# Kernel tuning notes

Measured on AMD Instinct MI355X. Metric: run time of the kernel, lower is better.

Reference implementation:

```python
import jax, jax.numpy as jnp
import numpy as np

B, T, N, C_IN, C_OUT, CHEB_K, ST_EMB = 8, 12, 2048, 64, 64, 2, 64


def setup_inputs() -> dict:
    key = jax.random.key(0)
    ks = jax.random.split(key, 9)
    inv = 1.0 / np.sqrt(ST_EMB)
    return {
        "x": jax.random.normal(ks[0], (B, T, N, C_IN), dtype=jnp.float32),
        "adj": jax.random.uniform(ks[1], (N, N), dtype=jnp.float32),
        "st_emb": jax.random.normal(ks[2], (T, 1, ST_EMB), dtype=jnp.float32),
        "weights": jax.random.normal(ks[3], (CHEB_K, C_IN, C_OUT), dtype=jnp.float32) * 0.02,
        "bias": jax.random.normal(ks[4], (C_OUT,), dtype=jnp.float32) * 0.02,
        "W1": jax.random.uniform(ks[5], (ST_EMB, 32), minval=-inv, maxval=inv, dtype=jnp.float32),
        "b1": jax.random.uniform(ks[6], (32,), minval=-inv, maxval=inv, dtype=jnp.float32),
        "W2": jax.random.uniform(ks[7], (32, 1), minval=-1/np.sqrt(32), maxval=1/np.sqrt(32), dtype=jnp.float32),
        "b2": jax.random.uniform(ks[8], (1,), minval=-1/np.sqrt(32), maxval=1/np.sqrt(32), dtype=jnp.float32),
    }


def reference(x, adj, st_emb, weights, bias, W1, b1, W2, b2):
    # lambda MLP: Linear -> ReLU -> Linear, then 1 + relu(.)
    h = jax.nn.relu(st_emb @ W1 + b1)            # [T,1,32]
    lam = 1.0 + jax.nn.relu(h @ W2 + b2)         # [T,1,1]
    c1 = (2.0 * lam - 2.0) / lam                 # [T,1,1] diagonal-scale coefficient
    c2 = 2.0 / lam                               # [T,1,1]
    # identity support einsum == per-time diagonal scaling of x
    x_g1 = c1[None] * x                          # [B,T,N,C]
    # adjacency support: scale factored out of the N x N contraction
    x_g2 = c2[None] * jnp.einsum('nm,btmc->btnc', adj, x)  # [B,T,N,C]
    x_g = jnp.stack([x_g1, x_g2], axis=3)        # [B,T,N,K,C]
    return jnp.einsum('btnki,kio->btno', x_g, weights) + bias
```

## Files before the change

kernel.cpp:

```cpp
#include <hip/hip_runtime.h>
#include <hip/hip_bf16.h>

#define B_ 8
#define T_ 12
#define N_ 2048
#define C_ 64
#define BM 128
#define BK 64

typedef __attribute__((ext_vector_type(4))) float f32x4;
typedef __attribute__((ext_vector_type(4))) __bf16 bf16x4;
typedef __attribute__((ext_vector_type(8))) __bf16 bf16x8;

#define GAS __attribute__((address_space(1)))
#define LAS __attribute__((address_space(3)))

static __device__ __forceinline__ void gld_lds16(const void* g, void* l) {
    __builtin_amdgcn_global_load_lds((const GAS void*)g, (LAS void*)l, 16, 0, 0);
}

#define WS_CBUF 0
#define WS_WTB  1024
#define WS_ADJB 32768
#define WS_XT   (32768 + 8388608)
#define WS_NEED ((size_t)(WS_XT) + 25165824)

__global__ void lam_kernel(const float* __restrict__ st, const float* __restrict__ W1,
                           const float* __restrict__ b1, const float* __restrict__ W2,
                           const float* __restrict__ b2, float* __restrict__ cbuf) {
    const int t = threadIdx.x >> 5;
    const int h = threadIdx.x & 31;
    if (t >= T_) return;
    float acc = b1[h];
    #pragma unroll 8
    for (int e = 0; e < 64; ++e) acc += st[t * 64 + e] * W1[e * 32 + h];
    float hv = fmaxf(acc, 0.f) * W2[h];
    #pragma unroll
    for (int off = 16; off; off >>= 1) hv += __shfl_down(hv, off, 32);
    if (h == 0) {
        float lam = 1.f + fmaxf(hv + b2[0], 0.f);
        cbuf[t]      = 2.f - 2.f / lam;
        cbuf[T_ + t] = 2.f / lam;
    }
}

__global__ void lamw_kernel(const float* __restrict__ st, const float* __restrict__ W1,
                            const float* __restrict__ b1, const float* __restrict__ W2,
                            const float* __restrict__ b2, const float* __restrict__ weights,
                            float* __restrict__ cbuf, __bf16* __restrict__ WtB) {
    const int t = threadIdx.x >> 5;
    const int h = threadIdx.x & 31;
    if (t < T_) {
        float acc = b1[h];
        #pragma unroll 8
        for (int e = 0; e < 64; ++e) acc += st[t * 64 + e] * W1[e * 32 + h];
        float hv = fmaxf(acc, 0.f) * W2[h];
        #pragma unroll
        for (int off = 16; off; off >>= 1) hv += __shfl_down(hv, off, 32);
        if (h == 0) {
            float lam = 1.f + fmaxf(hv + b2[0], 0.f);
            cbuf[t]      = 2.f - 2.f / lam;
            cbuf[T_ + t] = 2.f / lam;
        }
    }
    for (int e = threadIdx.x; e < 64 * 128; e += 512) {
        int o = e >> 7, k = e & 127;
        float v = (k < 64) ? weights[4096 + k * 64 + o] : weights[(k - 64) * 64 + o];
        WtB[o * 128 + k] = (__bf16)v;
    }
}

__global__ void cvt_fused(const float* __restrict__ x, __bf16* __restrict__ xT,
                          const float* __restrict__ adj, __bf16* __restrict__ adjb) {
    const int bid = blockIdx.x;
    const int tid = threadIdx.x;
    if (bid >= 3072) {
        const size_t i = ((size_t)(bid - 3072) * 256 + tid) * 8;
        const float4 f0 = *(const float4*)&adj[i];
        const float4 f1 = *(const float4*)&adj[i + 4];
        bf16x8 h = { (__bf16)f0.x, (__bf16)f0.y, (__bf16)f0.z, (__bf16)f0.w,
                     (__bf16)f1.x, (__bf16)f1.y, (__bf16)f1.z, (__bf16)f1.w };
        *(bf16x8*)&adjb[i] = h;
        return;
    }
    __shared__ __align__(16) __bf16 t[64][72];
    const int bt = bid >> 5, n0 = (bid & 31) * 64;
    {
        const int r = tid >> 2, c0 = (tid & 3) * 16;
        const float* src = x + ((size_t)bt * N_ + n0 + r) * C_ + c0;
        #pragma unroll
        for (int i = 0; i < 4; ++i) {
            float4 f = *(const float4*)(src + 4 * i);
            t[c0 + 4 * i + 0][r] = (__bf16)f.x;
            t[c0 + 4 * i + 1][r] = (__bf16)f.y;
            t[c0 + 4 * i + 2][r] = (__bf16)f.z;
            t[c0 + 4 * i + 3][r] = (__bf16)f.w;
        }
    }
    __syncthreads();
    {
        const int c = tid >> 2, nf = (tid & 3) * 16;
        __bf16* dst = xT + ((size_t)bt * C_ + c) * N_ + n0 + nf;
        *(bf16x8*)(dst)     = *(const bf16x8*)&t[c][nf];
        *(bf16x8*)(dst + 8) = *(const bf16x8*)&t[c][nf + 8];
    }
}

__global__ __launch_bounds__(256, 2) void dgcn_main2(
    const __bf16* __restrict__ adjb, const __bf16* __restrict__ xT,
    const float* __restrict__ x, const __bf16* __restrict__ WtB,
    const float* __restrict__ bias, const float* __restrict__ cbuf,
    float* __restrict__ out)
{
    __shared__ __align__(16) __bf16 smem[32768];
    char* sb = (char*)smem;

    const int m0  = blockIdx.x * BM;
    const int btg = blockIdx.y;
    const int tid = threadIdx.x;
    const int l   = tid & 63, w = tid >> 6;
    const int wr  = w >> 1, wc = w & 1;
    const int lr  = l & 15, lk = l >> 4;

    const __bf16* srcA[4];
    const __bf16* srcB[4];
    #pragma unroll
    for (int i = 0; i < 4; ++i) {
        int s = (w * 4 + i) * 64 + l;
        int r = s >> 3, j = s & 7;
        srcA[i] = adjb + (size_t)(m0 + r) * N_ + 8 * (j ^ (r & 7));
        int bb = s >> 9, c = (s >> 3) & 63;
        srcB[i] = xT + ((size_t)(btg * 2 + bb) * C_ + c) * N_ + 8 * (j ^ (c & 7));
    }

    f32x4 acc[4][4] = {};

    #pragma unroll
    for (int i = 0; i < 4; ++i) {
        gld_lds16(srcA[i], sb + (w * 4 + i) * 1024);
        gld_lds16(srcB[i], sb + 16384 + (w * 4 + i) * 1024);
    }

    int sel = 0;
    for (int kt = 0; kt < N_ / BK; ++kt) {
        __syncthreads();
        if (kt < N_ / BK - 1) {
            const int wo = (sel ^ 1) * 32768;
            #pragma unroll
            for (int i = 0; i < 4; ++i) {
                srcA[i] += BK;
                srcB[i] += BK;
                gld_lds16(srcA[i], sb + wo + (w * 4 + i) * 1024);
                gld_lds16(srcB[i], sb + wo + 16384 + (w * 4 + i) * 1024);
            }
        }
        const char* base = sb + sel * 32768;
        #pragma unroll
        for (int ks = 0; ks < 2; ++ks) {
            const int kb = ks * 64 + lk * 16;
            bf16x8 a[4];
            #pragma unroll
            for (int mi = 0; mi < 4; ++mi) {
                int rr = wr * 64 + mi * 16 + lr;
                a[mi] = *(const bf16x8*)(base + rr * 128 + (kb ^ ((rr & 7) << 4)));
            }
            #pragma unroll
            for (int nj = 0; nj < 4; ++nj) {
                int cc = nj * 16 + lr;
                bf16x8 b = *(const bf16x8*)(base + 16384 + wc * 8192 + cc * 128 + (kb ^ ((cc & 7) << 4)));
                #pragma unroll
                for (int mi = 0; mi < 4; ++mi)
                    acc[mi][nj] = __builtin_amdgcn_mfma_f32_16x16x32_bf16(a[mi], b, acc[mi][nj], 0, 0, 0);
            }
        }
        sel ^= 1;
    }

    #pragma unroll
    for (int bb = 0; bb < 2; ++bb) {
        const int btA = btg * 2 + bb;
        const int tloc = btA % T_;
        const float c1 = cbuf[tloc];
        const float c2 = cbuf[T_ + tloc];
        __syncthreads();
        if (wc == bb) {
            #pragma unroll
            for (int mi = 0; mi < 4; ++mi)
                #pragma unroll
                for (int nj = 0; nj < 4; ++nj)
                    #pragma unroll
                    for (int q = 0; q < 4; ++q) {
                        int row = wr * 64 + mi * 16 + lk * 4 + q;
                        int colb = (nj * 16 + lr) * 2;
                        *(__bf16*)(sb + row * 256 + (colb ^ ((row & 7) << 4))) =
                            (__bf16)(c2 * acc[mi][nj][q]);
                    }
        }
        {
            int row = w * 32 + (l >> 1);
            int c0 = (l & 1) * 32;
            const float* xs = x + ((size_t)btA * N_ + m0 + row) * C_ + c0;
            #pragma unroll
            for (int i = 0; i < 4; ++i) {
                float4 f0 = *(const float4*)(xs + 8 * i);
                float4 f1 = *(const float4*)(xs + 8 * i + 4);
                bf16x8 h = { (__bf16)(c1 * f0.x), (__bf16)(c1 * f0.y),
                             (__bf16)(c1 * f0.z), (__bf16)(c1 * f0.w),
                             (__bf16)(c1 * f1.x), (__bf16)(c1 * f1.y),
                             (__bf16)(c1 * f1.z), (__bf16)(c1 * f1.w) };
                int colb = 128 + c0 * 2 + 16 * i;
                *(bf16x8*)(sb + row * 256 + (colb ^ ((row & 7) << 4))) = h;
            }
        }
        __syncthreads();
        f32x4 oacc[2][4] = {};
        #pragma unroll
        for (int ks = 0; ks < 4; ++ks) {
            const int kb = ks * 64 + lk * 16;
            bf16x8 ea[2];
            #pragma unroll
            for (int mi2 = 0; mi2 < 2; ++mi2) {
                int row = w * 32 + mi2 * 16 + lr;
                ea[mi2] = *(const bf16x8*)(sb + row * 256 + (kb ^ ((row & 7) << 4)));
            }
            #pragma unroll
            for (int nj = 0; nj < 4; ++nj) {
                int o = nj * 16 + lr;
                bf16x8 bw = *(const bf16x8*)(WtB + o * 128 + ks * 32 + lk * 8);
                oacc[0][nj] = __builtin_amdgcn_mfma_f32_16x16x32_bf16(ea[0], bw, oacc[0][nj], 0, 0, 0);
                oacc[1][nj] = __builtin_amdgcn_mfma_f32_16x16x32_bf16(ea[1], bw, oacc[1][nj], 0, 0, 0);
            }
        }
        float* ob = out + (size_t)btA * N_ * C_;
        #pragma unroll
        for (int nj = 0; nj < 4; ++nj) {
            const float bv = bias[nj * 16 + lr];
            #pragma unroll
            for (int mi2 = 0; mi2 < 2; ++mi2)
                #pragma unroll
                for (int q = 0; q < 4; ++q) {
                    int row = w * 32 + mi2 * 16 + lk * 4 + q;
                    ob[(size_t)(m0 + row) * C_ + nj * 16 + lr] = oacc[mi2][nj][q] + bv;
                }
        }
    }
}

#define LDM 72
#define LDE 136
__global__ __launch_bounds__(256, 3) void dgcn_fb(
    const float* __restrict__ x, const float* __restrict__ adj,
    const float* __restrict__ weights, const float* __restrict__ bias,
    const float* __restrict__ cbuf, float* __restrict__ out)
{
    __shared__ __align__(16) __bf16 smem[BM * LDE];
    __shared__ __align__(16) __bf16 Wt[64 * LDE];
    __bf16* As = smem;
    __bf16* Bs = smem + BM * LDM;
    __bf16* E  = smem;

    const int mtile = blockIdx.x;
    const int bt    = blockIdx.y;
    const int tloc  = bt % T_;
    const int m0    = mtile * BM;
    const int tid   = threadIdx.x;
    const int lane  = tid & 63;
    const int w     = tid >> 6;

    const float c1 = cbuf[tloc];
    const float c2 = cbuf[T_ + tloc];
    const float* xbt = x + (size_t)bt * N_ * C_;

    for (int e = tid; e < 2 * 64 * 64; e += 256) {
        int kk = e >> 6, o = e & 63;
        float v = (kk < 64) ? weights[4096 + kk * 64 + o] : weights[(kk - 64) * 64 + o];
        Wt[o * LDE + kk] = (__bf16)v;
    }

    f32x4 acc[2][4] = {};
    const int c4 = tid & 15;
    const int rg = tid >> 4;
    const int lr = lane & 15;
    const int lk = lane >> 4;

    for (int kt = 0; kt < N_ / BK; ++kt) {
        const int k0 = kt * BK;
        __syncthreads();
        #pragma unroll
        for (int j = 0; j < 8; ++j) {
            const int r = rg + 16 * j;
            const float4 f = *(const float4*)&adj[(size_t)(m0 + r) * N_ + k0 + 4 * c4];
            bf16x4 h = { (__bf16)f.x, (__bf16)f.y, (__bf16)f.z, (__bf16)f.w };
            *(bf16x4*)&As[r * LDM + 4 * c4] = h;
        }
        #pragma unroll
        for (int j = 0; j < 4; ++j) {
            const int k  = (tid & 15) + 16 * j;
            const int c0 = 4 * (tid >> 4);
            const float4 f = *(const float4*)&xbt[(size_t)(k0 + k) * C_ + c0];
            Bs[(c0 + 0) * LDM + k] = (__bf16)f.x;
            Bs[(c0 + 1) * LDM + k] = (__bf16)f.y;
            Bs[(c0 + 2) * LDM + k] = (__bf16)f.z;
            Bs[(c0 + 3) * LDM + k] = (__bf16)f.w;
        }
        __syncthreads();
        #pragma unroll
        for (int ks = 0; ks < 2; ++ks) {
            bf16x8 a0 = *(const bf16x8*)&As[(w * 32 +  0 + lr) * LDM + ks * 32 + lk * 8];
            bf16x8 a1 = *(const bf16x8*)&As[(w * 32 + 16 + lr) * LDM + ks * 32 + lk * 8];
            #pragma unroll
            for (int nj = 0; nj < 4; ++nj) {
                bf16x8 b = *(const bf16x8*)&Bs[(nj * 16 + lr) * LDM + ks * 32 + lk * 8];
                acc[0][nj] = __builtin_amdgcn_mfma_f32_16x16x32_bf16(a0, b, acc[0][nj], 0, 0, 0);
                acc[1][nj] = __builtin_amdgcn_mfma_f32_16x16x32_bf16(a1, b, acc[1][nj], 0, 0, 0);
            }
        }
    }
    __syncthreads();

    #pragma unroll
    for (int j = 0; j < 8; ++j) {
        const int r = rg + 16 * j;
        const float4 f = *(const float4*)&xbt[(size_t)(m0 + r) * C_ + 4 * c4];
        bf16x4 h = { (__bf16)(c1 * f.x), (__bf16)(c1 * f.y), (__bf16)(c1 * f.z), (__bf16)(c1 * f.w) };
        *(bf16x4*)&E[r * LDE + 64 + 4 * c4] = h;
    }
    #pragma unroll
    for (int mi = 0; mi < 2; ++mi)
        #pragma unroll
        for (int nj = 0; nj < 4; ++nj)
            #pragma unroll
            for (int q = 0; q < 4; ++q) {
                const int row = w * 32 + mi * 16 + lk * 4 + q;
                const int col = nj * 16 + lr;
                E[row * LDE + col] = (__bf16)(c2 * acc[mi][nj][q]);
            }
    __syncthreads();

    f32x4 oacc[2][4] = {};
    #pragma unroll
    for (int ks = 0; ks < 4; ++ks) {
        bf16x8 a0 = *(const bf16x8*)&E[(w * 32 +  0 + lr) * LDE + ks * 32 + lk * 8];
        bf16x8 a1 = *(const bf16x8*)&E[(w * 32 + 16 + lr) * LDE + ks * 32 + lk * 8];
        #pragma unroll
        for (int nj = 0; nj < 4; ++nj) {
            bf16x8 bw = *(const bf16x8*)&Wt[(nj * 16 + lr) * LDE + ks * 32 + lk * 8];
            oacc[0][nj] = __builtin_amdgcn_mfma_f32_16x16x32_bf16(a0, bw, oacc[0][nj], 0, 0, 0);
            oacc[1][nj] = __builtin_amdgcn_mfma_f32_16x16x32_bf16(a1, bw, oacc[1][nj], 0, 0, 0);
        }
    }
    float* obt = out + (size_t)bt * N_ * C_;
    #pragma unroll
    for (int nj = 0; nj < 4; ++nj) {
        const float bv = bias[nj * 16 + lr];
        #pragma unroll
        for (int mi = 0; mi < 2; ++mi)
            #pragma unroll
            for (int q = 0; q < 4; ++q) {
                const int row = w * 32 + mi * 16 + lk * 4 + q;
                obt[(size_t)(m0 + row) * C_ + nj * 16 + lr] = oacc[mi][nj][q] + bv;
            }
    }
}

extern "C" void kernel_launch(void* const* d_in, const int* in_sizes, int n_in,
                              void* d_out, int out_size, void* d_ws, size_t ws_size,
                              hipStream_t stream) {
    const float* x       = (const float*)d_in[0];
    const float* adj     = (const float*)d_in[1];
    const float* st_emb  = (const float*)d_in[2];
    const float* weights = (const float*)d_in[3];
    const float* bias    = (const float*)d_in[4];
    const float* W1      = (const float*)d_in[5];
    const float* b1      = (const float*)d_in[6];
    const float* W2      = (const float*)d_in[7];
    const float* b2      = (const float*)d_in[8];
    float* out = (float*)d_out;
    char* ws = (char*)d_ws;
    float* cbuf = (float*)(ws + WS_CBUF);

    if (ws_size >= WS_NEED) {
        __bf16* WtB  = (__bf16*)(ws + WS_WTB);
        __bf16* adjb = (__bf16*)(ws + WS_ADJB);
        __bf16* xT   = (__bf16*)(ws + WS_XT);
        lamw_kernel<<<1, 512, 0, stream>>>(st_emb, W1, b1, W2, b2, weights, cbuf, WtB);
        cvt_fused<<<5120, 256, 0, stream>>>(x, xT, adj, adjb);
        dgcn_main2<<<dim3(N_ / BM, B_ * T_ / 2), 256, 0, stream>>>(adjb, xT, x, WtB, bias, cbuf, out);
    } else {
        lam_kernel<<<1, 384, 0, stream>>>(st_emb, W1, b1, W2, b2, cbuf);
        dgcn_fb<<<dim3(N_ / BM, B_ * T_), 256, 0, stream>>>(x, adj, weights, bias, cbuf, out);
    }
}
```

Baseline: 99.15 us.

## Reassociate graph conv: apply weights before adjacency GEMM, fuse epilogue

Uses associativity to compute P1 = x·W1 and P0 = c1·x·W0 + bias in the conversion kernel, so the large adjacency GEMM multiplies adj by the projected P1 (stored transposed in bf16) and the epilogue simply adds c2·acc to P0. This removes the second per-tile MFMA stage and the LDS staging of the concatenated feature tile. The main GEMM now covers three bt slices per block (N=192) with a larger LDS buffer, and P0 is held in bf16 or fp32 depending on workspace size. The trade-off is extra rounding from bf16 P1 and P0, plus a larger LDS footprint that may reduce occupancy.

```diff
diff --git a/kernel.cpp b/kernel.cpp
--- a/kernel.cpp
+++ b/kernel.cpp
@@ -22,8 +22,10 @@
 #define WS_CBUF 0
 #define WS_WTB  1024
 #define WS_ADJB 32768
-#define WS_XT   (32768 + 8388608)
-#define WS_NEED ((size_t)(WS_XT) + 25165824)
+#define WS_P1T  (32768 + 8388608)
+#define WS_P0S  (WS_P1T + 25165824)
+#define WS_MID  ((size_t)WS_P0S)
+#define WS_FULL ((size_t)WS_P0S + 25165824)
 
 __global__ void lam_kernel(const float* __restrict__ st, const float* __restrict__ W1,
                            const float* __restrict__ b1, const float* __restrict__ W2,
@@ -70,12 +72,17 @@
     }
 }
 
-__global__ void cvt_fused(const float* __restrict__ x, __bf16* __restrict__ xT,
-                          const float* __restrict__ adj, __bf16* __restrict__ adjb) {
+template<bool FULLP>
+__global__ __launch_bounds__(256, 4) void pcvt_kernel(
+    const float* __restrict__ x, const float* __restrict__ adj,
+    const __bf16* __restrict__ WtB, const float* __restrict__ cbuf,
+    const float* __restrict__ bias, __bf16* __restrict__ adjb,
+    __bf16* __restrict__ P1T, __bf16* __restrict__ P0S, float* __restrict__ out)
+{
     const int bid = blockIdx.x;
     const int tid = threadIdx.x;
-    if (bid >= 3072) {
-        const size_t i = ((size_t)(bid - 3072) * 256 + tid) * 8;
+    if (bid >= 1536) {
+        const size_t i = ((size_t)(bid - 1536) * 256 + tid) * 8;
         const float4 f0 = *(const float4*)&adj[i];
         const float4 f1 = *(const float4*)&adj[i + 4];
         bf16x8 h = { (__bf16)f0.x, (__bf16)f0.y, (__bf16)f0.z, (__bf16)f0.w,
@@ -83,36 +90,81 @@
         *(bf16x8*)&adjb[i] = h;
         return;
     }
-    __shared__ __align__(16) __bf16 t[64][72];
-    const int bt = bid >> 5, n0 = (bid & 31) * 64;
-    {
-        const int r = tid >> 2, c0 = (tid & 3) * 16;
-        const float* src = x + ((size_t)bt * N_ + n0 + r) * C_ + c0;
-        #pragma unroll
-        for (int i = 0; i < 4; ++i) {
-            float4 f = *(const float4*)(src + 4 * i);
-            t[c0 + 4 * i + 0][r] = (__bf16)f.x;
-            t[c0 + 4 * i + 1][r] = (__bf16)f.y;
-            t[c0 + 4 * i + 2][r] = (__bf16)f.z;
-            t[c0 + 4 * i + 3][r] = (__bf16)f.w;
-        }
+    __shared__ __align__(16) __bf16 T[64 * 128];
+    char* TB = (char*)T;
+    const int bt = bid >> 4, n0 = (bid & 15) * 128;
+    const int l = tid & 63, w = tid >> 6;
+    const int lr = l & 15, lk = l >> 4;
+    const float c1 = cbuf[bt % T_];
+
+    f32x4 p1[2][4] = {}, p0[2][4] = {};
+    #pragma unroll
+    for (int ks = 0; ks < 2; ++ks) {
+        bf16x8 a[2];
+        #pragma unroll
+        for (int mi = 0; mi < 2; ++mi) {
+            const float* xs = x + ((size_t)bt * N_ + n0 + w * 32 + mi * 16 + lr) * C_ + ks * 32 + lk * 8;
+            float4 f0 = *(const float4*)xs;
+            float4 f1 = *(const float4*)(xs + 4);
+            a[mi] = { (__bf16)f0.x, (__bf16)f0.y, (__bf16)f0.z, (__bf16)f0.w,
+                      (__bf16)f1.x, (__bf16)f1.y, (__bf16)f1.z, (__bf16)f1.w };
+        }
+        #pragma unroll
+        for (int nj = 0; nj < 4; ++nj) {
+            const __bf16* wb = WtB + (nj * 16 + lr) * 128 + ks * 32 + lk * 8;
+            bf16x8 b1v = *(const bf16x8*)wb;
+            bf16x8 b0v = *(const bf16x8*)(wb + 64);
+            #pragma unroll
+            for (int mi = 0; mi < 2; ++mi) {
+                p1[mi][nj] = __builtin_amdgcn_mfma_f32_16x16x32_bf16(a[mi], b1v, p1[mi][nj], 0, 0, 0);
+                p0[mi][nj] = __builtin_amdgcn_mfma_f32_16x16x32_bf16(a[mi], b0v, p0[mi][nj], 0, 0, 0);
+            }
+        }
+    }
+    #pragma unroll
+    for (int nj = 0; nj < 4; ++nj) {
+        const int o = nj * 16 + lr;
+        const float bv = bias[o];
+        #pragma unroll
+        for (int mi = 0; mi < 2; ++mi)
+            #pragma unroll
+            for (int q = 0; q < 4; ++q) {
+                const int row = w * 32 + mi * 16 + lk * 4 + q;
+                const size_t idx = ((size_t)bt * N_ + n0 + row) * C_ + o;
+                const float v = c1 * p0[mi][nj][q] + bv;
+                if (FULLP) P0S[idx] = (__bf16)v; else out[idx] = v;
+            }
+    }
+    #pragma unroll
+    for (int nj = 0; nj < 4; ++nj) {
+        const int o = nj * 16 + lr;
+        #pragma unroll
+        for (int mi = 0; mi < 2; ++mi)
+            #pragma unroll
+            for (int q = 0; q < 4; ++q) {
+                const int row = w * 32 + mi * 16 + lk * 4 + q;
+                *(__bf16*)(TB + o * 256 + ((row * 2) ^ ((o & 7) << 4))) = (__bf16)p1[mi][nj][q];
+            }
     }
     __syncthreads();
     {
-        const int c = tid >> 2, nf = (tid & 3) * 16;
-        __bf16* dst = xT + ((size_t)bt * C_ + c) * N_ + n0 + nf;
-        *(bf16x8*)(dst)     = *(const bf16x8*)&t[c][nf];
-        *(bf16x8*)(dst + 8) = *(const bf16x8*)&t[c][nf + 8];
-    }
-}
-
-__global__ __launch_bounds__(256, 2) void dgcn_main2(
-    const __bf16* __restrict__ adjb, const __bf16* __restrict__ xT,
-    const float* __restrict__ x, const __bf16* __restrict__ WtB,
-    const float* __restrict__ bias, const float* __restrict__ cbuf,
+        const int o = tid >> 2, seg = tid & 3;
+        __bf16* dst = P1T + ((size_t)bt * 64 + o) * N_ + n0 + seg * 32;
+        #pragma unroll
+        for (int i = 0; i < 4; ++i) {
+            const int chunk = seg * 64 + i * 16;
+            *(bf16x8*)(dst + i * 8) = *(const bf16x8*)(TB + o * 256 + (chunk ^ ((o & 7) << 4)));
+        }
+    }
+}
+
+template<bool FULLP>
+__global__ __launch_bounds__(256, 2) void dgcn_main3(
+    const __bf16* __restrict__ adjb, const __bf16* __restrict__ P1T,
+    const __bf16* __restrict__ P0S, const float* __restrict__ cbuf,
     float* __restrict__ out)
 {
-    __shared__ __align__(16) __bf16 smem[32768];
+    __shared__ __align__(16) __bf16 smem[40960];
     char* sb = (char*)smem;
 
     const int m0  = blockIdx.x * BM;
@@ -123,38 +175,45 @@
     const int lr  = l & 15, lk = l >> 4;
 
     const __bf16* srcA[4];
-    const __bf16* srcB[4];
+    const __bf16* srcB[6];
     #pragma unroll
     for (int i = 0; i < 4; ++i) {
         int s = (w * 4 + i) * 64 + l;
         int r = s >> 3, j = s & 7;
         srcA[i] = adjb + (size_t)(m0 + r) * N_ + 8 * (j ^ (r & 7));
-        int bb = s >> 9, c = (s >> 3) & 63;
-        srcB[i] = xT + ((size_t)(btg * 2 + bb) * C_ + c) * N_ + 8 * (j ^ (c & 7));
-    }
-
-    f32x4 acc[4][4] = {};
-
-    #pragma unroll
-    for (int i = 0; i < 4; ++i) {
-        gld_lds16(srcA[i], sb + (w * 4 + i) * 1024);
-        gld_lds16(srcB[i], sb + 16384 + (w * 4 + i) * 1024);
-    }
+    }
+    #pragma unroll
+    for (int i = 0; i < 6; ++i) {
+        int s = (w * 6 + i) * 64 + l;
+        int btl = s >> 9, rem = s & 511;
+        int o = rem >> 3, j = rem & 7;
+        srcB[i] = P1T + ((size_t)(btg * 3 + btl) * 64 + o) * N_ + 8 * (j ^ (o & 7));
+    }
+
+    f32x4 acc[4][6] = {};
+
+    #pragma unroll
+    for (int i = 0; i < 4; ++i) gld_lds16(srcA[i], sb + (w * 4 + i) * 1024);
+    #pragma unroll
+    for (int i = 0; i < 6; ++i) gld_lds16(srcB[i], sb + 16384 + (w * 6 + i) * 1024);
 
     int sel = 0;
     for (int kt = 0; kt < N_ / BK; ++kt) {
         __syncthreads();
         if (kt < N_ / BK - 1) {
-            const int wo = (sel ^ 1) * 32768;
+            const int wo = (sel ^ 1) * 40960;
             #pragma unroll
             for (int i = 0; i < 4; ++i) {
                 srcA[i] += BK;
+                gld_lds16(srcA[i], sb + wo + (w * 4 + i) * 1024);
+            }
+            #pragma unroll
+            for (int i = 0; i < 6; ++i) {
                 srcB[i] += BK;
-                gld_lds16(srcA[i], sb + wo + (w * 4 + i) * 1024);
-                gld_lds16(srcB[i], sb + wo + 16384 + (w * 4 + i) * 1024);
-            }
-        }
-        const char* base = sb + sel * 32768;
+                gld_lds16(srcB[i], sb + wo + 16384 + (w * 6 + i) * 1024);
+            }
+        }
+        const char* base = sb + sel * 40960;
         #pragma unroll
         for (int ks = 0; ks < 2; ++ks) {
             const int kb = ks * 64 + lk * 16;
@@ -165,9 +224,10 @@
                 a[mi] = *(const bf16x8*)(base + rr * 128 + (kb ^ ((rr & 7) << 4)));
             }
             #pragma unroll
-            for (int nj = 0; nj < 4; ++nj) {
-                int cc = nj * 16 + lr;
-                bf16x8 b = *(const bf16x8*)(base + 16384 + wc * 8192 + cc * 128 + (kb ^ ((cc & 7) << 4)));
+            for (int nj = 0; nj < 6; ++nj) {
+                int c = wc * 96 + nj * 16 + lr;
+                int btl = c >> 6, o = c & 63;
+                bf16x8 b = *(const bf16x8*)(base + 16384 + btl * 8192 + o * 128 + (kb ^ ((o & 7) << 4)));
                 #pragma unroll
                 for (int mi = 0; mi < 4; ++mi)
                     acc[mi][nj] = __builtin_amdgcn_mfma_f32_16x16x32_bf16(a[mi], b, acc[mi][nj], 0, 0, 0);
@@ -177,72 +237,20 @@
     }
 
     #pragma unroll
-    for (int bb = 0; bb < 2; ++bb) {
-        const int btA = btg * 2 + bb;
-        const int tloc = btA % T_;
-        const float c1 = cbuf[tloc];
-        const float c2 = cbuf[T_ + tloc];
-        __syncthreads();
-        if (wc == bb) {
-            #pragma unroll
-            for (int mi = 0; mi < 4; ++mi)
-                #pragma unroll
-                for (int nj = 0; nj < 4; ++nj)
-                    #pragma unroll
-                    for (int q = 0; q < 4; ++q) {
-                        int row = wr * 64 + mi * 16 + lk * 4 + q;
-                        int colb = (nj * 16 + lr) * 2;
-                        *(__bf16*)(sb + row * 256 + (colb ^ ((row & 7) << 4))) =
-                            (__bf16)(c2 * acc[mi][nj][q]);
-                    }
-        }
-        {
-            int row = w * 32 + (l >> 1);
-            int c0 = (l & 1) * 32;
-            const float* xs = x + ((size_t)btA * N_ + m0 + row) * C_ + c0;
-            #pragma unroll
-            for (int i = 0; i < 4; ++i) {
-                float4 f0 = *(const float4*)(xs + 8 * i);
-                float4 f1 = *(const float4*)(xs + 8 * i + 4);
-                bf16x8 h = { (__bf16)(c1 * f0.x), (__bf16)(c1 * f0.y),
-                             (__bf16)(c1 * f0.z), (__bf16)(c1 * f0.w),
-                             (__bf16)(c1 * f1.x), (__bf16)(c1 * f1.y),
-                             (__bf16)(c1 * f1.z), (__bf16)(c1 * f1.w) };
-                int colb = 128 + c0 * 2 + 16 * i;
-                *(bf16x8*)(sb + row * 256 + (colb ^ ((row & 7) << 4))) = h;
-            }
-        }
-        __syncthreads();
-        f32x4 oacc[2][4] = {};
-        #pragma unroll
-        for (int ks = 0; ks < 4; ++ks) {
-            const int kb = ks * 64 + lk * 16;
-            bf16x8 ea[2];
-            #pragma unroll
-            for (int mi2 = 0; mi2 < 2; ++mi2) {
-                int row = w * 32 + mi2 * 16 + lr;
-                ea[mi2] = *(const bf16x8*)(sb + row * 256 + (kb ^ ((row & 7) << 4)));
-            }
-            #pragma unroll
-            for (int nj = 0; nj < 4; ++nj) {
-                int o = nj * 16 + lr;
-                bf16x8 bw = *(const bf16x8*)(WtB + o * 128 + ks * 32 + lk * 8);
-                oacc[0][nj] = __builtin_amdgcn_mfma_f32_16x16x32_bf16(ea[0], bw, oacc[0][nj], 0, 0, 0);
-                oacc[1][nj] = __builtin_amdgcn_mfma_f32_16x16x32_bf16(ea[1], bw, oacc[1][nj], 0, 0, 0);
-            }
-        }
-        float* ob = out + (size_t)btA * N_ * C_;
-        #pragma unroll
-        for (int nj = 0; nj < 4; ++nj) {
-            const float bv = bias[nj * 16 + lr];
-            #pragma unroll
-            for (int mi2 = 0; mi2 < 2; ++mi2)
-                #pragma unroll
-                for (int q = 0; q < 4; ++q) {
-                    int row = w * 32 + mi2 * 16 + lk * 4 + q;
-                    ob[(size_t)(m0 + row) * C_ + nj * 16 + lr] = oacc[mi2][nj][q] + bv;
-                }
-        }
+    for (int nj = 0; nj < 6; ++nj) {
+        const int c = wc * 96 + nj * 16 + lr;
+        const int btl = c >> 6, o = c & 63;
+        const int btA = btg * 3 + btl;
+        const float c2 = cbuf[T_ + (btA % T_)];
+        #pragma unroll
+        for (int mi = 0; mi < 4; ++mi)
+            #pragma unroll
+            for (int q = 0; q < 4; ++q) {
+                const int row = wr * 64 + mi * 16 + lk * 4 + q;
+                const size_t idx = ((size_t)btA * N_ + m0 + row) * C_ + o;
+                const float p0v = FULLP ? (float)P0S[idx] : out[idx];
+                out[idx] = c2 * acc[mi][nj][q] + p0v;
+            }
     }
 }
 
@@ -379,13 +387,19 @@
     char* ws = (char*)d_ws;
     float* cbuf = (float*)(ws + WS_CBUF);
 
-    if (ws_size >= WS_NEED) {
+    if (ws_size >= WS_MID) {
         __bf16* WtB  = (__bf16*)(ws + WS_WTB);
         __bf16* adjb = (__bf16*)(ws + WS_ADJB);
-        __bf16* xT   = (__bf16*)(ws + WS_XT);
+        __bf16* P1T  = (__bf16*)(ws + WS_P1T);
+        __bf16* P0S  = (__bf16*)(ws + WS_P0S);
         lamw_kernel<<<1, 512, 0, stream>>>(st_emb, W1, b1, W2, b2, weights, cbuf, WtB);
-        cvt_fused<<<5120, 256, 0, stream>>>(x, xT, adj, adjb);
-        dgcn_main2<<<dim3(N_ / BM, B_ * T_ / 2), 256, 0, stream>>>(adjb, xT, x, WtB, bias, cbuf, out);
+        if (ws_size >= WS_FULL) {
+            pcvt_kernel<true><<<3584, 256, 0, stream>>>(x, adj, WtB, cbuf, bias, adjb, P1T, P0S, out);
+            dgcn_main3<true><<<dim3(N_ / BM, 32), 256, 0, stream>>>(adjb, P1T, P0S, cbuf, out);
+        } else {
+            pcvt_kernel<false><<<3584, 256, 0, stream>>>(x, adj, WtB, cbuf, bias, adjb, P1T, P0S, out);
+            dgcn_main3<false><<<dim3(N_ / BM, 32), 256, 0, stream>>>(adjb, P1T, P0S, cbuf, out);
+        }
     } else {
         lam_kernel<<<1, 384, 0, stream>>>(st_emb, W1, b1, W2, b2, cbuf);
         dgcn_fb<<<dim3(N_ / BM, B_ * T_), 256, 0, stream>>>(x, adj, weights, bias, cbuf, out);
```

New measurement: 95.58 us. 3.6% less time.
